# Performance work log

Measured on AMD Instinct MI355X. Metric: run time of the kernel, lower is better.

Reference implementation:

```python
import jax, jax.numpy as jnp
import numpy as np

B, S, D = 4, 4096, 64

def setup_inputs() -> dict:
    key = jax.random.key(0)
    kq, kk, kv = jax.random.split(key, 3)
    q = jax.random.normal(kq, (B, S, D), dtype=jnp.float32)
    k = jax.random.normal(kk, (B, S, D), dtype=jnp.float32)
    v = jax.random.normal(kv, (B, S, D), dtype=jnp.float32)
    return {"q": q, "k": k, "v": v}

def reference(q, k, v):
    # unnormalized attention: scores [b,i,j], then weighted sum over j
    attn = jnp.einsum('bid,bjd->bij', q, k)
    out = jnp.einsum('bij,bjd->bid', attn, v)
    return out
```

## Files before the change

kernel.cpp:

```cpp
#include <hip/hip_runtime.h>
#include <hip/hip_bf16.h>


#define BATCH 4
#define SEQ   4096
#define DIM   64
#define NCH   64
#define CHUNK 64

typedef float f4  __attribute__((ext_vector_type(4)));
typedef short bf16x8 __attribute__((ext_vector_type(8)));
typedef float f32x4  __attribute__((ext_vector_type(4)));

__device__ inline unsigned short f2bf(float f) {
    union { float f; unsigned u; } v; v.f = f;
    unsigned r = (v.u + 0x7fffu + ((v.u >> 16) & 1u)) >> 16;
    return (unsigned short)r;
}

__global__ __launch_bounds__(256) void k1_partial(const float* __restrict__ K,
                                                  const float* __restrict__ V,
                                                  float* __restrict__ part) {
    __shared__ f4 Ks[1024];
    __shared__ f4 Vs[1024];
    const int bx = blockIdx.x;
    const int t  = threadIdx.x;
    const f4* Kg = (const f4*)(K + (size_t)bx * (CHUNK * DIM));
    const f4* Vg = (const f4*)(V + (size_t)bx * (CHUNK * DIM));
#pragma unroll
    for (int i = 0; i < 4; ++i) {
        Ks[t + 256 * i] = Kg[t + 256 * i];
        Vs[t + 256 * i] = Vg[t + 256 * i];
    }
    __syncthreads();
    const int rg = t >> 4;
    const int cg = t & 15;
    f4 acc0 = 0.f, acc1 = 0.f, acc2 = 0.f, acc3 = 0.f;
#pragma unroll 8
    for (int j = 0; j < CHUNK; ++j) {
        f4 a = Ks[j * 16 + rg];
        f4 v = Vs[j * 16 + cg];
        acc0 += v * a.x;
        acc1 += v * a.y;
        acc2 += v * a.z;
        acc3 += v * a.w;
    }
    f4* P = (f4*)part + (size_t)bx * 1024;
    P[(rg * 4 + 0) * 16 + cg] = acc0;
    P[(rg * 4 + 1) * 16 + cg] = acc1;
    P[(rg * 4 + 2) * 16 + cg] = acc2;
    P[(rg * 4 + 3) * 16 + cg] = acc3;
}

__global__ __launch_bounds__(256) void k2_reduce(const float* __restrict__ part,
                                                 unsigned short* __restrict__ MB) {
    const int tg = blockIdx.x * 256 + threadIdx.x;
    const int b = tg >> 12;
    const int e = tg & 4095;
    float s = 0.f;
#pragma unroll 8
    for (int p = 0; p < NCH; ++p)
        s += part[((size_t)(b * NCH + p)) * 4096 + e];
    const int dp = e >> 6;
    const int c  = e & 63;
    const int ct = c >> 4, m = c & 15;
    const int ks = dp >> 5, quad = (dp >> 3) & 3, j = dp & 7;
    const int idx = (((b * 8 + ct * 2 + ks) * 64) + quad * 16 + m) * 8 + j;
    MB[idx] = f2bf(s);
}

__global__ __launch_bounds__(256) void k3_qm(const float* __restrict__ Q,
                                             const unsigned short* __restrict__ MB,
                                             float* __restrict__ out) {
    const int bx = blockIdx.x;
    const int t  = threadIdx.x;
    const int wave = t >> 6, lane = t & 63;
    const int m = lane & 15, quad = lane >> 4;
    const int b = bx >> 6;
    const int row0 = (bx & 63) * 64 + wave * 16;

    const float* qrow = Q + ((size_t)b * SEQ + row0 + m) * DIM;
    bf16x8 afrag[2];
#pragma unroll
    for (int ks = 0; ks < 2; ++ks) {
        const f4* qp = (const f4*)(qrow + ks * 32 + quad * 8);
        f4 q1 = qp[0], q2 = qp[1];
        bf16x8 a;
        a[0] = (short)f2bf(q1.x); a[1] = (short)f2bf(q1.y);
        a[2] = (short)f2bf(q1.z); a[3] = (short)f2bf(q1.w);
        a[4] = (short)f2bf(q2.x); a[5] = (short)f2bf(q2.y);
        a[6] = (short)f2bf(q2.z); a[7] = (short)f2bf(q2.w);
        afrag[ks] = a;
    }

    const bf16x8* MBv = (const bf16x8*)MB + (size_t)b * 8 * 64;
    f32x4 acc[4];
#pragma unroll
    for (int ct = 0; ct < 4; ++ct) { acc[ct] = (f32x4)0.f; }
#pragma unroll
    for (int ct = 0; ct < 4; ++ct) {
#pragma unroll
        for (int ks = 0; ks < 2; ++ks) {
            bf16x8 bfrag = MBv[(ct * 2 + ks) * 64 + lane];
            acc[ct] = __builtin_amdgcn_mfma_f32_16x16x32_bf16(afrag[ks], bfrag, acc[ct], 0, 0, 0);
        }
    }

    float* orow = out + ((size_t)b * SEQ + row0) * DIM;
#pragma unroll
    for (int ct = 0; ct < 4; ++ct) {
#pragma unroll
        for (int r = 0; r < 4; ++r) {
            orow[(quad * 4 + r) * DIM + ct * 16 + m] = acc[ct][r];
        }
    }
}

extern "C" void kernel_launch(void* const* d_in, const int* in_sizes, int n_in,
                              void* d_out, int out_size, void* d_ws, size_t ws_size,
                              hipStream_t stream) {
    const float* q = (const float*)d_in[0];
    const float* k = (const float*)d_in[1];
    const float* v = (const float*)d_in[2];
    float* out = (float*)d_out;

    float* part = (float*)d_ws;
    unsigned short* MB = (unsigned short*)((char*)d_ws + (size_t)4 * 1024 * 1024);

    k1_partial<<<BATCH * NCH, 256, 0, stream>>>(k, v, part);
    k2_reduce<<<64, 256, 0, stream>>>(part, MB);
    k3_qm<<<BATCH * NCH, 256, 0, stream>>>(q, MB, out);
}
```

Before: 74.24 us.

## Fuse three attention kernels into one cooperative kernel with grid syncs

Measured after the change: 136.9 us. 1.84x slower.

```diff
diff --git a/kernel.cpp b/kernel.cpp
--- a/kernel.cpp
+++ b/kernel.cpp
@@ -1,5 +1,6 @@
 #include <hip/hip_runtime.h>
 #include <hip/hip_bf16.h>
+#include <hip/hip_cooperative_groups.h>
 
 
 #define BATCH 4
@@ -8,6 +9,8 @@
 #define NCH   64
 #define CHUNK 64
 
+namespace cg = cooperative_groups;
+
 typedef float f4  __attribute__((ext_vector_type(4)));
 typedef short bf16x8 __attribute__((ext_vector_type(8)));
 typedef float f32x4  __attribute__((ext_vector_type(4)));
@@ -16,6 +19,120 @@
     union { float f; unsigned u; } v; v.f = f;
     unsigned r = (v.u + 0x7fffu + ((v.u >> 16) & 1u)) >> 16;
     return (unsigned short)r;
+}
+
+__global__ __launch_bounds__(256) void fused_attn(const float* __restrict__ Q,
+                                                  const float* __restrict__ K,
+                                                  const float* __restrict__ V,
+                                                  float* __restrict__ out,
+                                                  float* __restrict__ part,
+                                                  unsigned short* __restrict__ MB) {
+    __shared__ f4 Ks[1024];
+    __shared__ f4 Vs[1024];
+    const int bx = blockIdx.x;
+    const int t  = threadIdx.x;
+
+    const int wave = t >> 6, lane = t & 63;
+    const int m = lane & 15, quad = lane >> 4;
+    const int b = bx >> 6;
+    const int row0 = (bx & 63) * 64 + wave * 16;
+    const float* qrow = Q + ((size_t)b * SEQ + row0 + m) * DIM;
+    const f4* qp0 = (const f4*)(qrow + quad * 8);
+    const f4* qp1 = (const f4*)(qrow + 32 + quad * 8);
+    f4 q0a = qp0[0], q0b = qp0[1];
+    f4 q1a = qp1[0], q1b = qp1[1];
+
+    {
+        const f4* Kg = (const f4*)(K + (size_t)bx * (CHUNK * DIM));
+        const f4* Vg = (const f4*)(V + (size_t)bx * (CHUNK * DIM));
+#pragma unroll
+        for (int i = 0; i < 4; ++i) {
+            Ks[t + 256 * i] = Kg[t + 256 * i];
+            Vs[t + 256 * i] = Vg[t + 256 * i];
+        }
+        __syncthreads();
+        const int rg = t >> 4;
+        const int cgi = t & 15;
+        f4 a0 = 0.f, a1 = 0.f, a2 = 0.f, a3 = 0.f;
+#pragma unroll 8
+        for (int j = 0; j < CHUNK; ++j) {
+            f4 a = Ks[j * 16 + rg];
+            f4 v = Vs[j * 16 + cgi];
+            a0 += v * a.x;
+            a1 += v * a.y;
+            a2 += v * a.z;
+            a3 += v * a.w;
+        }
+        f4* P = (f4*)part + (size_t)bx * 1024;
+        P[(rg * 4 + 0) * 16 + cgi] = a0;
+        P[(rg * 4 + 1) * 16 + cgi] = a1;
+        P[(rg * 4 + 2) * 16 + cgi] = a2;
+        P[(rg * 4 + 3) * 16 + cgi] = a3;
+    }
+
+    cg::this_grid().sync();
+
+    {
+        const int g   = bx * 256 + t;
+        const int e   = g >> 2;
+        const int sub = g & 3;
+        const int eb  = e >> 12;
+        const int idx = e & 4095;
+        const float* pp = part + ((size_t)(eb * NCH + sub * 16)) * 4096 + idx;
+        float s = 0.f;
+#pragma unroll
+        for (int p = 0; p < 16; ++p) s += pp[(size_t)p * 4096];
+        s += __shfl_xor(s, 1);
+        s += __shfl_xor(s, 2);
+        if (sub == 0) {
+            const int dp = idx >> 6;
+            const int c  = idx & 63;
+            const int ct = c >> 4, mm = c & 15;
+            const int ks = dp >> 5, qd = (dp >> 3) & 3, j = dp & 7;
+            MB[(((eb * 8 + ct * 2 + ks) * 64) + qd * 16 + mm) * 8 + j] = f2bf(s);
+        }
+    }
+
+    cg::this_grid().sync();
+
+    {
+        bf16x8 afrag[2];
+        {
+            bf16x8 a;
+            a[0] = (short)f2bf(q0a.x); a[1] = (short)f2bf(q0a.y);
+            a[2] = (short)f2bf(q0a.z); a[3] = (short)f2bf(q0a.w);
+            a[4] = (short)f2bf(q0b.x); a[5] = (short)f2bf(q0b.y);
+            a[6] = (short)f2bf(q0b.z); a[7] = (short)f2bf(q0b.w);
+            afrag[0] = a;
+            a[0] = (short)f2bf(q1a.x); a[1] = (short)f2bf(q1a.y);
+            a[2] = (short)f2bf(q1a.z); a[3] = (short)f2bf(q1a.w);
+            a[4] = (short)f2bf(q1b.x); a[5] = (short)f2bf(q1b.y);
+            a[6] = (short)f2bf(q1b.z); a[7] = (short)f2bf(q1b.w);
+            afrag[1] = a;
+        }
+
+        const bf16x8* MBv = (const bf16x8*)MB + (size_t)b * 8 * 64;
+        f32x4 acc[4];
+#pragma unroll
+        for (int ct = 0; ct < 4; ++ct) acc[ct] = (f32x4)0.f;
+#pragma unroll
+        for (int ct = 0; ct < 4; ++ct) {
+#pragma unroll
+            for (int ks = 0; ks < 2; ++ks) {
+                bf16x8 bfrag = MBv[(ct * 2 + ks) * 64 + lane];
+                acc[ct] = __builtin_amdgcn_mfma_f32_16x16x32_bf16(afrag[ks], bfrag, acc[ct], 0, 0, 0);
+            }
+        }
+
+        float* orow = out + ((size_t)b * SEQ + row0) * DIM;
+#pragma unroll
+        for (int ct = 0; ct < 4; ++ct) {
+#pragma unroll
+            for (int r = 0; r < 4; ++r) {
+                orow[(quad * 4 + r) * DIM + ct * 16 + m] = acc[ct][r];
+            }
+        }
+    }
 }
 
 __global__ __launch_bounds__(256) void k1_partial(const float* __restrict__ K,
@@ -33,23 +150,19 @@
         Vs[t + 256 * i] = Vg[t + 256 * i];
     }
     __syncthreads();
-    const int rg = t >> 4;
-    const int cg = t & 15;
-    f4 acc0 = 0.f, acc1 = 0.f, acc2 = 0.f, acc3 = 0.f;
+    const int rg = t >> 4, cgi = t & 15;
+    f4 a0 = 0.f, a1 = 0.f, a2 = 0.f, a3 = 0.f;
 #pragma unroll 8
     for (int j = 0; j < CHUNK; ++j) {
         f4 a = Ks[j * 16 + rg];
-        f4 v = Vs[j * 16 + cg];
-        acc0 += v * a.x;
-        acc1 += v * a.y;
-        acc2 += v * a.z;
-        acc3 += v * a.w;
+        f4 v = Vs[j * 16 + cgi];
+        a0 += v * a.x; a1 += v * a.y; a2 += v * a.z; a3 += v * a.w;
     }
     f4* P = (f4*)part + (size_t)bx * 1024;
-    P[(rg * 4 + 0) * 16 + cg] = acc0;
-    P[(rg * 4 + 1) * 16 + cg] = acc1;
-    P[(rg * 4 + 2) * 16 + cg] = acc2;
-    P[(rg * 4 + 3) * 16 + cg] = acc3;
+    P[(rg * 4 + 0) * 16 + cgi] = a0;
+    P[(rg * 4 + 1) * 16 + cgi] = a1;
+    P[(rg * 4 + 2) * 16 + cgi] = a2;
+    P[(rg * 4 + 3) * 16 + cgi] = a3;
 }
 
 __global__ __launch_bounds__(256) void k2_reduce(const float* __restrict__ part,
@@ -63,10 +176,9 @@
         s += part[((size_t)(b * NCH + p)) * 4096 + e];
     const int dp = e >> 6;
     const int c  = e & 63;
-    const int ct = c >> 4, m = c & 15;
-    const int ks = dp >> 5, quad = (dp >> 3) & 3, j = dp & 7;
-    const int idx = (((b * 8 + ct * 2 + ks) * 64) + quad * 16 + m) * 8 + j;
-    MB[idx] = f2bf(s);
+    const int ct = c >> 4, mm = c & 15;
+    const int ks = dp >> 5, qd = (dp >> 3) & 3, j = dp & 7;
+    MB[(((b * 8 + ct * 2 + ks) * 64) + qd * 16 + mm) * 8 + j] = f2bf(s);
 }
 
 __global__ __launch_bounds__(256) void k3_qm(const float* __restrict__ Q,
@@ -96,7 +208,7 @@
     const bf16x8* MBv = (const bf16x8*)MB + (size_t)b * 8 * 64;
     f32x4 acc[4];
 #pragma unroll
-    for (int ct = 0; ct < 4; ++ct) { acc[ct] = (f32x4)0.f; }
+    for (int ct = 0; ct < 4; ++ct) acc[ct] = (f32x4)0.f;
 #pragma unroll
     for (int ct = 0; ct < 4; ++ct) {
 #pragma unroll
@@ -127,7 +239,13 @@
     float* part = (float*)d_ws;
     unsigned short* MB = (unsigned short*)((char*)d_ws + (size_t)4 * 1024 * 1024);
 
-    k1_partial<<<BATCH * NCH, 256, 0, stream>>>(k, v, part);
-    k2_reduce<<<64, 256, 0, stream>>>(part, MB);
-    k3_qm<<<BATCH * NCH, 256, 0, stream>>>(q, MB, out);
-}
+    void* args[] = { (void*)&q, (void*)&k, (void*)&v, (void*)&out, (void*)&part, (void*)&MB };
+    hipError_t err = hipLaunchCooperativeKernel((const void*)&fused_attn,
+                                                dim3(BATCH * NCH), dim3(256),
+                                                args, 0, stream);
+    if (err != hipSuccess) {
+        k1_partial<<<BATCH * NCH, 256, 0, stream>>>(k, v, part);
+        k2_reduce<<<64, 256, 0, stream>>>(part, MB);
+        k3_qm<<<BATCH * NCH, 256, 0, stream>>>(q, MB, out);
+    }
+}
```
